# Optimization experiments

Hardware: AMD Instinct MI355X
Metric: run time of the kernel (lower is better)

The kernel has to match this reference:

```python
import jax, jax.numpy as jnp
import numpy as np

N = 50000     # num_nodes
E = 600000    # num_edges
H = 128       # h_dim
OUT = 32      # out_dim
R = 64        # num_rels
B = 16        # num_bases


def setup_inputs() -> dict:
    key = jax.random.key(0)
    ks = jax.random.split(key, 11)
    src = jax.random.randint(ks[0], (E,), 0, N)
    dst = jax.random.randint(ks[1], (E,), 0, N)
    etype = jax.random.randint(ks[2], (E,), 0, R)
    norm = jax.random.uniform(ks[3], (E, 1), dtype=jnp.float32)  # edge norm (e.g. 1/deg)
    emb = jax.random.normal(ks[4], (N, H), dtype=jnp.float32) * 0.05
    # basis-decomposed relation weights: W_r = sum_b comp[r,b] * V[b]
    V1 = jax.random.normal(ks[5], (B, H, H), dtype=jnp.float32) * (1.0 / np.sqrt(H))
    comp1 = jax.random.normal(ks[6], (R, B), dtype=jnp.float32) * (1.0 / np.sqrt(B))
    bias1 = jnp.zeros((H,), dtype=jnp.float32)
    V2 = jax.random.normal(ks[7], (B, H, OUT), dtype=jnp.float32) * (1.0 / np.sqrt(H))
    comp2 = jax.random.normal(ks[8], (R, B), dtype=jnp.float32) * (1.0 / np.sqrt(B))
    bias2 = jnp.zeros((OUT,), dtype=jnp.float32)
    return {"src": src, "dst": dst, "etype": etype, "norm": norm, "emb": emb,
            "V1": V1, "comp1": comp1, "bias1": bias1,
            "V2": V2, "comp2": comp2, "bias2": bias2}


def _rel_graph_conv(x, src, dst, etype, norm, V, comp, bias):
    # message for edge e: (x[src_e] @ W_{etype_e}) * norm_e, W_r = sum_b comp[r,b] V_b.
    # Since W is linear, fold norm into the gathered features, and aggregate
    # per (dst, basis) BEFORE the dense basis matmul (aggregate-first trick):
    #   agg[v, b] = sum_{e: dst_e=v} comp[etype_e, b] * norm_e * x[src_e]
    #   out[v]    = sum_b agg[v, b] @ V_b + bias
    xs = x[src] * norm                      # [E, in]
    w = comp[etype]                         # [E, B] per-edge basis coefficients
    # loop over the small fixed basis count (B=16), reusing the [E, in] buffer
    agg = jnp.stack(
        [jax.ops.segment_sum(xs * w[:, b:b + 1], dst, num_segments=N) for b in range(B)],
        axis=1,
    )                                       # [N, B, in]
    return jnp.einsum('nbi,bio->no', agg, V) + bias


def reference(src, dst, etype, norm, emb, V1, comp1, bias1, V2, comp2, bias2):
    h = _rel_graph_conv(emb, src, dst, etype, norm, V1, comp1, bias1)
    h = jax.nn.relu(h)                      # dropout p=0.0 -> identity
    h = _rel_graph_conv(h, src, dst, etype, norm, V2, comp2, bias2)
    return h
```

## Files before the change

kernel.cpp:

```cpp
#include <hip/hip_runtime.h>
#include <hip/hip_bf16.h>

#define NN 50000
#define EE 600000
#define HH 128
#define OUTD 32
#define RR 64
#define BB 16
#define KK 2048
#define SC_B ((NN + 1023) / 1024)

typedef short s16x8 __attribute__((ext_vector_type(8)));
typedef float f32x4 __attribute__((ext_vector_type(4)));
typedef float f32x2 __attribute__((ext_vector_type(2)));
typedef unsigned short ushort_t;
typedef unsigned int uint_t;

__device__ inline ushort_t f_to_bf16(float f){
    __hip_bfloat16 h = __float2bfloat16(f);
    return *reinterpret_cast<ushort_t*>(&h);
}
__device__ inline uint_t pack_bf16x2(float a, float b){
    return (uint_t)f_to_bf16(a) | ((uint_t)f_to_bf16(b) << 16);
}

__global__ void zero_i32(int* p, int n){
    int i = blockIdx.x*256 + threadIdx.x;
    if (i < n) p[i] = 0;
}

__global__ void hist_kernel(const int* __restrict__ dst, int* counts){
    int e = blockIdx.x*256 + threadIdx.x;
    if (e < EE) atomicAdd(&counts[dst[e]], 1);
}

__global__ void scan_part(const int* __restrict__ counts, int* __restrict__ tot){
    int b = blockIdx.x, t = threadIdx.x;
    int i0 = b*1024 + t*4;
    int s = 0;
    if (i0 + 3 < NN){
        int4 v = *reinterpret_cast<const int4*>(&counts[i0]);
        s = v.x + v.y + v.z + v.w;
    } else {
        for (int j = 0; j < 4; j++) if (i0 + j < NN) s += counts[i0 + j];
    }
    #pragma unroll
    for (int off = 32; off; off >>= 1) s += __shfl_xor(s, off, 64);
    __shared__ int ws[4];
    if ((t & 63) == 0) ws[t >> 6] = s;
    __syncthreads();
    if (t == 0) tot[b] = ws[0] + ws[1] + ws[2] + ws[3];
}

__global__ void scan_tot(int* tot){
    int t = threadIdx.x;
    int v = (t < SC_B) ? tot[t] : 0;
    int x = v;
    #pragma unroll
    for (int off = 1; off < 64; off <<= 1){
        int y = __shfl_up(x, off, 64);
        if (t >= off) x += y;
    }
    if (t < SC_B) tot[t] = x - v;
}

__global__ void scan_final(const int* __restrict__ counts, const int* __restrict__ tot,
                           int* __restrict__ offsets, int* __restrict__ cursor){
    int b = blockIdx.x, t = threadIdx.x, lane = t & 63, wv = t >> 6;
    int i0 = b*1024 + t*4;
    int v[4]; int s = 0;
    #pragma unroll
    for (int j = 0; j < 4; j++){ v[j] = (i0 + j < NN) ? counts[i0 + j] : 0; s += v[j]; }
    int x = s;
    #pragma unroll
    for (int off = 1; off < 64; off <<= 1){
        int y = __shfl_up(x, off, 64);
        if (lane >= off) x += y;
    }
    __shared__ int ws[4];
    if (lane == 63) ws[wv] = x;
    __syncthreads();
    int pre = tot[b];
    for (int i = 0; i < wv; i++) pre += ws[i];
    int run = pre + x - s;
    #pragma unroll
    for (int j = 0; j < 4; j++){
        if (i0 + j < NN){
            cursor[i0 + j] = run;
            offsets[i0 + j + 1] = run + v[j];
        }
        run += v[j];
    }
    if (b == 0 && t == 0) offsets[0] = 0;
}

__global__ void scatter_kernel(const int* __restrict__ dst, const int* __restrict__ src,
                               const int* __restrict__ etype, const float* __restrict__ norm,
                               int* cursor, int* __restrict__ msrc, int* __restrict__ netn){
    int e = blockIdx.x*256 + threadIdx.x;
    if (e >= EE) return;
    int d = dst[e];
    int r = atomicAdd(&cursor[d], 1);
    msrc[r] = src[e];
    netn[r] = (__float_as_int(norm[e]) & ~63) | etype[e];
}

__global__ void convw_kernel(const float* __restrict__ V1, const float* __restrict__ V2,
                             ushort_t* __restrict__ Wt1, ushort_t* __restrict__ Wt2){
    int i = blockIdx.x*256 + threadIdx.x;
    if (i < HH*KK){
        int o = i / KK, k = i % KK;
        Wt1[i] = f_to_bf16(V1[(size_t)k*HH + o]);
    } else {
        int j = i - HH*KK;
        if (j < OUTD*KK){
            int o = j / KK, k = j % KK;
            Wt2[j] = f_to_bf16(V2[(size_t)k*OUTD + o]);
        }
    }
}

__global__ void conv_emb(const float* __restrict__ emb, ushort_t* __restrict__ xb){
    int i = blockIdx.x*256 + threadIdx.x;
    if (i < NN*HH/2){
        float2 f = *reinterpret_cast<const float2*>(emb + 2*(size_t)i);
        *reinterpret_cast<uint_t*>(xb + 2*(size_t)i) = pack_bf16x2(f.x, f.y);
    }
}

__global__ __launch_bounds__(256, 8) void agg_kernel(
    const ushort_t* __restrict__ xin, const int* __restrict__ msrc,
    const int* __restrict__ netn, const int* __restrict__ offsets,
    const float* __restrict__ comp, ushort_t* __restrict__ agg,
    int v0, int vc)
{
    int w = threadIdx.x >> 6, lane = threadIdx.x & 63;
    int v = v0 + blockIdx.x*4 + w;
    if (v >= v0 + vc) return;
    int p0 = offsets[v];
    int dd = offsets[v+1] - p0;
    const uint_t* xrow = reinterpret_cast<const uint_t*>(xin);

    f32x2 accA[8], accB[8];
    #pragma unroll
    for (int bp = 0; bp < 8; bp++){
        accA[bp].x = 0.f; accA[bp].y = 0.f;
        accB[bp].x = 0.f; accB[bp].y = 0.f;
    }

    for (int c0 = 0; c0 < dd; c0 += 64){
        int nc = min(64, dd - c0);
        int li = p0 + c0 + min(lane, nc - 1);
        int mp = msrc[li];
        int nr = netn[li];
        uint_t xr[8];
        #pragma unroll
        for (int j = 0; j < 8; ++j){
            int sr = __builtin_amdgcn_readlane(mp, min(j, nc - 1));
            xr[j] = xrow[(size_t)sr*64 + lane];
        }
        for (int eb = 0; eb < nc; eb += 8){
            #pragma unroll
            for (int j = 0; j < 8; ++j){
                int e = eb + j;
                int ec = min(e, nc - 1);
                int nb = __builtin_amdgcn_readlane(nr, ec);
                int et = nb & 63;
                float nw = (e < nc) ? __int_as_float(nb & ~63) : 0.f;
                uint_t u = xr[j];
                f32x2 xs;
                xs.x = __uint_as_float(u << 16) * nw;
                xs.y = __uint_as_float(u & 0xffff0000u) * nw;
                int en = e + 8;
                if (en < nc){
                    int srn = __builtin_amdgcn_readlane(mp, en);
                    xr[j] = xrow[(size_t)srn*64 + lane];
                }
                const f32x2* cp = reinterpret_cast<const f32x2*>(comp + et*BB);
                #pragma unroll
                for (int bp = 0; bp < 8; bp++){
                    f32x2 c2 = cp[bp];
                    asm("v_pk_fma_f32 %0, %1, %2, %0 op_sel:[0,0,0] op_sel_hi:[1,0,1]"
                        : "+v"(accA[bp]) : "s"(c2), "v"(xs));
                    asm("v_pk_fma_f32 %0, %1, %2, %0 op_sel:[0,1,0] op_sel_hi:[1,1,1]"
                        : "+v"(accB[bp]) : "s"(c2), "v"(xs));
                }
            }
        }
    }
    uint_t* arow = reinterpret_cast<uint_t*>(agg) + (size_t)(v - v0)*1024 + lane;
    #pragma unroll
    for (int b = 0; b < BB; b++)
        arow[b*64] = pack_bf16x2(accA[b>>1][b&1], accB[b>>1][b&1]);
}

template<int BN, bool RELU, bool OUT_BF16>
__global__ __launch_bounds__(512, 6) void gemm_kernel(
    const ushort_t* __restrict__ A, const ushort_t* __restrict__ Wt,
    const float* __restrict__ bias, void* __restrict__ yout, int vc)
{
    __shared__ ushort_t Alds[64][72];
    __shared__ ushort_t Blds[BN][72];
    constexpr int CT = BN / 32;
    int tid = threadIdx.x, lane = tid & 63, lane15 = lane & 15;
    int w = tid >> 6, wr = w >> 1, wc = w & 1;
    int m0 = blockIdx.x * 64;
    int kc8 = (lane >> 4) * 8;

    f32x4 acc[CT];
    #pragma unroll
    for (int ct = 0; ct < CT; ct++)
        #pragma unroll
        for (int j = 0; j < 4; j++) acc[ct][j] = 0.f;

    for (int k0 = 0; k0 < KK; k0 += 64){
        {
            int row = tid >> 3, kc = (tid & 7) * 8;
            uint4 val = make_uint4(0u,0u,0u,0u);
            if (m0 + row < vc)
                val = *reinterpret_cast<const uint4*>(A + (size_t)(m0+row)*KK + k0 + kc);
            *reinterpret_cast<uint4*>(&Alds[row][kc]) = val;
        }
        if (BN == 128){
            #pragma unroll
            for (int i = 0; i < 2; i++){
                int idx = tid + i*512;
                int row = idx >> 3, kc = (idx & 7)*8;
                *reinterpret_cast<uint4*>(&Blds[row][kc]) =
                    *reinterpret_cast<const uint4*>(Wt + (size_t)row*KK + k0 + kc);
            }
        } else {
            if (tid < BN*8){
                int row = tid >> 3, kc = (tid & 7)*8;
                *reinterpret_cast<uint4*>(&Blds[row][kc]) =
                    *reinterpret_cast<const uint4*>(Wt + (size_t)row*KK + k0 + kc);
            }
        }
        __syncthreads();
        #pragma unroll
        for (int ks = 0; ks < 2; ks++){
            s16x8 a = *reinterpret_cast<const s16x8*>(&Alds[wr*16 + lane15][ks*32 + kc8]);
            #pragma unroll
            for (int ct = 0; ct < CT; ct++){
                s16x8 b = *reinterpret_cast<const s16x8*>(
                    &Blds[wc*(BN/2) + ct*16 + lane15][ks*32 + kc8]);
                acc[ct] = __builtin_amdgcn_mfma_f32_16x16x32_bf16(a, b, acc[ct], 0,0,0);
            }
        }
        __syncthreads();
    }
    int rb = m0 + wr*16 + ((lane >> 4) << 2);
    #pragma unroll
    for (int ct = 0; ct < CT; ct++){
        int col = wc*(BN/2) + ct*16 + lane15;
        float bv = bias[col];
        #pragma unroll
        for (int r = 0; r < 4; r++){
            int row = rb + r;
            if (row < vc){
                float val = acc[ct][r] + bv;
                if (RELU) val = fmaxf(val, 0.f);
                if (OUT_BF16)
                    reinterpret_cast<ushort_t*>(yout)[(size_t)row*BN + col] = f_to_bf16(val);
                else
                    reinterpret_cast<float*>(yout)[(size_t)row*BN + col] = val;
            }
        }
    }
}

extern "C" void kernel_launch(void* const* d_in, const int* in_sizes, int n_in,
                              void* d_out, int out_size, void* d_ws, size_t ws_size,
                              hipStream_t stream){
    const int*   src   = (const int*)d_in[0];
    const int*   dst   = (const int*)d_in[1];
    const int*   etype = (const int*)d_in[2];
    const float* norm  = (const float*)d_in[3];
    const float* emb   = (const float*)d_in[4];
    const float* V1    = (const float*)d_in[5];
    const float* comp1 = (const float*)d_in[6];
    const float* bias1 = (const float*)d_in[7];
    const float* V2    = (const float*)d_in[8];
    const float* comp2 = (const float*)d_in[9];
    const float* bias2 = (const float*)d_in[10];
    float* out = (float*)d_out;

    char* w = (char*)d_ws;
    auto alloc = [&](size_t bytes) -> char* {
        char* p = w; w += (bytes + 255) & ~(size_t)255; return p;
    };
    int*      offsets = (int*)alloc((NN + 1) * 4);
    int*      counts  = (int*)alloc(NN * 4);
    int*      cursor  = (int*)alloc(NN * 4);
    int*      tot     = (int*)alloc(SC_B * 4);
    int*      msrc    = (int*)alloc((size_t)EE * 4);
    int*      netn    = (int*)alloc((size_t)EE * 4);
    ushort_t* Wt1     = (ushort_t*)alloc((size_t)HH * KK * 2);
    ushort_t* Wt2     = (ushort_t*)alloc((size_t)OUTD * KK * 2);
    ushort_t* xb      = (ushort_t*)alloc((size_t)NN * HH * 2);
    ushort_t* h       = (ushort_t*)alloc((size_t)NN * HH * 2);
    size_t used  = (size_t)(w - (char*)d_ws);
    size_t avail = ws_size > used ? ws_size - used : 0;
    int chunkN = (int)(avail / ((size_t)KK * 2));
    chunkN &= ~63;
    if (chunkN < 64) chunkN = 64;
    if (chunkN > NN) chunkN = NN;
    ushort_t* agg = (ushort_t*)w;

    zero_i32<<<(NN + 255)/256, 256, 0, stream>>>(counts, NN);
    hist_kernel<<<(EE + 255)/256, 256, 0, stream>>>(dst, counts);
    scan_part<<<SC_B, 256, 0, stream>>>(counts, tot);
    scan_tot<<<1, 64, 0, stream>>>(tot);
    scan_final<<<SC_B, 256, 0, stream>>>(counts, tot, offsets, cursor);
    scatter_kernel<<<(EE + 255)/256, 256, 0, stream>>>(dst, src, etype, norm,
                                                       cursor, msrc, netn);
    convw_kernel<<<((HH + OUTD)*KK + 255)/256, 256, 0, stream>>>(V1, V2, Wt1, Wt2);
    conv_emb<<<(NN*HH/2 + 255)/256, 256, 0, stream>>>(emb, xb);

    for (int v0 = 0; v0 < NN; v0 += chunkN){
        int vc = (NN - v0 < chunkN) ? (NN - v0) : chunkN;
        agg_kernel<<<(vc + 3)/4, 256, 0, stream>>>(
            xb, msrc, netn, offsets, comp1, agg, v0, vc);
        gemm_kernel<HH, true, true><<<(vc + 63)/64, 512, 0, stream>>>(
            agg, Wt1, bias1, h + (size_t)v0 * HH, vc);
    }
    for (int v0 = 0; v0 < NN; v0 += chunkN){
        int vc = (NN - v0 < chunkN) ? (NN - v0) : chunkN;
        agg_kernel<<<(vc + 3)/4, 256, 0, stream>>>(
            h, msrc, netn, offsets, comp2, agg, v0, vc);
        gemm_kernel<OUTD, false, false><<<(vc + 63)/64, 512, 0, stream>>>(
            agg, Wt2, bias2, out + (size_t)v0 * OUTD, vc);
    }
}
```

Before: 324.5 us.

## Double-buffer GEMM tiles with direct global-to-LDS loads and XOR swizzle

Reworks the basis GEMM main loop to stage A and B tiles straight from global memory into LDS with global_load_lds, into two alternating buffers, so the next K tile loads while MFMAs run on the current one. It replaces the padded LDS layout with an XOR-swizzled 128-byte row layout to avoid bank conflicts, and clamps out-of-range rows instead of zero-filling them. This cuts register round-trips and one barrier per iteration. It relies on the async load completing at the barrier without an explicit vmcnt wait, and it doubles LDS use, which may lower occupancy.

```diff
diff --git a/kernel.cpp b/kernel.cpp
--- a/kernel.cpp
+++ b/kernel.cpp
@@ -15,6 +15,8 @@
 typedef float f32x2 __attribute__((ext_vector_type(2)));
 typedef unsigned short ushort_t;
 typedef unsigned int uint_t;
+typedef __attribute__((address_space(3))) uint_t lds_u32;
+typedef const __attribute__((address_space(1))) uint_t glb_u32;
 
 __device__ inline ushort_t f_to_bf16(float f){
     __hip_bfloat16 h = __float2bfloat16(f);
@@ -199,13 +201,34 @@
     const ushort_t* __restrict__ A, const ushort_t* __restrict__ Wt,
     const float* __restrict__ bias, void* __restrict__ yout, int vc)
 {
-    __shared__ ushort_t Alds[64][72];
-    __shared__ ushort_t Blds[BN][72];
+    __shared__ __align__(16) char Ald[2][64*128];
+    __shared__ __align__(16) char Bld[2][BN*128];
     constexpr int CT = BN / 32;
     int tid = threadIdx.x, lane = tid & 63, lane15 = lane & 15;
     int w = tid >> 6, wr = w >> 1, wc = w & 1;
     int m0 = blockIdx.x * 64;
-    int kc8 = (lane >> 4) * 8;
+
+    int sr_ = tid >> 3, sj_ = (tid & 7) ^ (sr_ & 7);
+    const ushort_t* agp = A + (size_t)(m0 + min(sr_, vc - 1))*KK + sj_*8;
+    const ushort_t* bgp0 = Wt + (size_t)sr_*KK + sj_*8;
+    const ushort_t* bgp1 = Wt + (size_t)(64 + sr_)*KK + sj_*8;
+
+    auto stage = [&](int buf){
+        __builtin_amdgcn_global_load_lds((glb_u32*)agp,
+            (lds_u32*)(&Ald[buf][w*1024]), 16, 0, 0);
+        if constexpr (BN == 128){
+            __builtin_amdgcn_global_load_lds((glb_u32*)bgp0,
+                (lds_u32*)(&Bld[buf][w*1024]), 16, 0, 0);
+            __builtin_amdgcn_global_load_lds((glb_u32*)bgp1,
+                (lds_u32*)(&Bld[buf][8192 + w*1024]), 16, 0, 0);
+            bgp1 += 64;
+        } else {
+            if (w < 4)
+                __builtin_amdgcn_global_load_lds((glb_u32*)bgp0,
+                    (lds_u32*)(&Bld[buf][w*1024]), 16, 0, 0);
+        }
+        agp += 64; bgp0 += 64;
+    };
 
     f32x4 acc[CT];
     #pragma unroll
@@ -213,42 +236,32 @@
         #pragma unroll
         for (int j = 0; j < 4; j++) acc[ct][j] = 0.f;
 
-    for (int k0 = 0; k0 < KK; k0 += 64){
-        {
-            int row = tid >> 3, kc = (tid & 7) * 8;
-            uint4 val = make_uint4(0u,0u,0u,0u);
-            if (m0 + row < vc)
-                val = *reinterpret_cast<const uint4*>(A + (size_t)(m0+row)*KK + k0 + kc);
-            *reinterpret_cast<uint4*>(&Alds[row][kc]) = val;
-        }
-        if (BN == 128){
-            #pragma unroll
-            for (int i = 0; i < 2; i++){
-                int idx = tid + i*512;
-                int row = idx >> 3, kc = (idx & 7)*8;
-                *reinterpret_cast<uint4*>(&Blds[row][kc]) =
-                    *reinterpret_cast<const uint4*>(Wt + (size_t)row*KK + k0 + kc);
-            }
-        } else {
-            if (tid < BN*8){
-                int row = tid >> 3, kc = (tid & 7)*8;
-                *reinterpret_cast<uint4*>(&Blds[row][kc]) =
-                    *reinterpret_cast<const uint4*>(Wt + (size_t)row*KK + k0 + kc);
-            }
-        }
-        __syncthreads();
+    int arow = wr*16 + lane15;
+    auto compute = [&](int buf){
         #pragma unroll
         for (int ks = 0; ks < 2; ks++){
-            s16x8 a = *reinterpret_cast<const s16x8*>(&Alds[wr*16 + lane15][ks*32 + kc8]);
+            int csw = (ks*4 + (lane >> 4)) ^ (lane15 & 7);
+            s16x8 a = *reinterpret_cast<const s16x8*>(&Ald[buf][arow*128 + csw*16]);
             #pragma unroll
             for (int ct = 0; ct < CT; ct++){
-                s16x8 b = *reinterpret_cast<const s16x8*>(
-                    &Blds[wc*(BN/2) + ct*16 + lane15][ks*32 + kc8]);
+                int brow = wc*(BN/2) + ct*16 + lane15;
+                s16x8 b = *reinterpret_cast<const s16x8*>(&Bld[buf][brow*128 + csw*16]);
                 acc[ct] = __builtin_amdgcn_mfma_f32_16x16x32_bf16(a, b, acc[ct], 0,0,0);
             }
         }
+    };
+
+    stage(0);
+    __syncthreads();
+    for (int t = 0; t < KK/64; t += 2){
+        if (t + 1 < KK/64) stage(1);
+        compute(0);
         __syncthreads();
-    }
+        if (t + 2 < KK/64) stage(0);
+        compute(1);
+        __syncthreads();
+    }
+
     int rb = m0 + wr*16 + ((lane >> 4) << 2);
     #pragma unroll
     for (int ct = 0; ct < CT; ct++){
```

New measurement: 319.1 us. About the same (-1.6%).
